# Kernel optimization log

Hardware: AMD Instinct MI355X
Metric: run time of the kernel (lower is better)

## Reference

```python
import jax, jax.numpy as jnp
import numpy as np
from jax import lax

N_HEAD = 16
SEQ = 2048
EMB = 512
D = SEQ // N_HEAD  # input_dim = 128
KSIZE = 3
EPS = 1e-5  # BatchNorm1d default eps


def setup_inputs() -> dict:
    key = jax.random.key(0)
    ks = jax.random.split(key, 5)
    inputs = jax.random.normal(ks[0], (8, SEQ, EMB), jnp.float32)
    # grouped Conv1d: groups = D, weight shape (out_ch, in_ch/groups, k) = (512, 4, 3)
    conv_w = jax.random.normal(ks[1], (EMB, EMB // D, KSIZE), jnp.float32) * 0.1
    conv_b = jax.random.normal(ks[2], (EMB,), jnp.float32) * 0.1
    gamma = jnp.ones((EMB,), jnp.float32)
    beta = jnp.zeros((EMB,), jnp.float32)
    lin_w = jax.random.normal(ks[3], (D, D), jnp.float32) * (1.0 / np.sqrt(D))
    lin_b = jax.random.normal(ks[4], (D,), jnp.float32) * 0.1
    return {"inputs": inputs, "conv_w": conv_w, "conv_b": conv_b,
            "gamma": gamma, "beta": beta, "lin_w": lin_w, "lin_b": lin_b}


def reference(inputs, conv_w, conv_b, gamma, beta, lin_w, lin_b):
    b = inputs.shape[0]
    # nlp mode: (b, S, E) -> (b*n_head, E, D)
    x = inputs.reshape(-1, EMB, D)

    # local information: grouped Conv1d (stride 1, padding 1, groups=D) + residual, GELU, BatchNorm (training stats)
    conv = lax.conv_general_dilated(
        x, conv_w, window_strides=(1,), padding=[(1, 1)],
        dimension_numbers=("NCH", "OIH", "NCH"), feature_group_count=D,
    ) + conv_b[None, :, None]
    q = jax.nn.gelu(conv + x, approximate=False)
    mu = q.mean(axis=(0, 2), keepdims=True)
    var = q.var(axis=(0, 2), keepdims=True)  # biased, as torch BN uses for normalization
    q = gamma[None, :, None] * (q - mu) * lax.rsqrt(var + EPS) + beta[None, :, None]

    # bernoulli sampling with prob=1 -> all-ones mask -> plain softmax over dim=-2 (the E axis)
    k = jax.nn.gelu(jax.nn.softmax(x, axis=1), approximate=False)

    # global information: Linear(D, D) on last dim, then GELU
    v = jax.nn.gelu(jnp.einsum("bed,od->beo", x, lin_w) + lin_b, approximate=False)

    # attention: (B', E, D) x (B', D, E) -> (B', E, E), softmax over last dim
    attn = jax.nn.softmax(
        jnp.einsum("bed,bfd->bef", q, k) / np.float32(np.sqrt(EMB)), axis=-1
    )
    out = jnp.einsum("bef,bfd->bed", attn, v)  # (B', E, D)
    return out.reshape(b, SEQ, EMB), attn
```

## Files before the change

### kernel.cpp

```cpp
#include <hip/hip_runtime.h>
#include <math.h>

#define Bn   128
#define Ech  512
#define Dd   128
#define NCNT 16384

typedef __bf16 bf16;
typedef __attribute__((ext_vector_type(8))) __bf16 bf16x8;
typedef __attribute__((ext_vector_type(4))) __bf16 bf16x4;
typedef __attribute__((ext_vector_type(4))) float f32x4;

__device__ __forceinline__ float gelu_exact(float x) {
    return 0.5f * x * (1.0f + erff(x * 0.70710678118654752f));
}

static __device__ __forceinline__ f32x4 mfma16(bf16x8 a, bf16x8 b, f32x4 c) {
    return __builtin_amdgcn_mfma_f32_16x16x32_bf16(a, b, c, 0, 0, 0);
}

__device__ __forceinline__ void stage_tile_bf16(const bf16* __restrict__ src,
                                                int src_ld, bf16* __restrict__ lds,
                                                int t)
{
    #pragma unroll
    for (int p = 0; p < 4; p++) {
        const int idx = t + 256 * p;
        const int row = idx >> 4;
        const int k16 = idx & 15;
        const float4 v = *(const float4*)((const char*)src +
                          (size_t)row * src_ld * 2 + k16 * 16);
        const unsigned byte = (unsigned)(row * 256 + k16 * 16) ^ ((row & 7) << 4);
        *(float4*)((char*)lds + byte) = v;
    }
}

__device__ __forceinline__ void stage_tile_f32(const float* __restrict__ src,
                                               int src_ld, bf16* __restrict__ lds,
                                               int t)
{
    #pragma unroll
    for (int p = 0; p < 4; p++) {
        const int idx = t + 256 * p;
        const int row = idx >> 4;
        const int k16 = idx & 15;
        const float4 a = *(const float4*)(src + (size_t)row * src_ld + k16 * 8);
        const float4 b = *(const float4*)(src + (size_t)row * src_ld + k16 * 8 + 4);
        bf16x8 o;
        o[0] = (bf16)a.x; o[1] = (bf16)a.y; o[2] = (bf16)a.z; o[3] = (bf16)a.w;
        o[4] = (bf16)b.x; o[5] = (bf16)b.y; o[6] = (bf16)b.z; o[7] = (bf16)b.w;
        const unsigned byte = (unsigned)(row * 256 + k16 * 16) ^ ((row & 7) << 4);
        *(bf16x8*)((char*)lds + byte) = o;
    }
}

__device__ __forceinline__ bf16x8 frag(const bf16* __restrict__ lds, int row, int koff)
{
    const unsigned byte = (unsigned)(row * 256 + koff * 2) ^ ((row & 7) << 4);
    return *(const bf16x8*)((const char*)lds + byte);
}

__global__ __launch_bounds__(256) void k_conv_gelu_stats(
    const float* __restrict__ x, const float* __restrict__ cw,
    const float* __restrict__ cb, bf16* __restrict__ qpre,
    float* __restrict__ csum, float* __restrict__ csumsq)
{
    __shared__ float xt[64 * 128];
    const int n  = blockIdx.y;
    const int c0 = blockIdx.x * 64;
    const float* xb = x + (size_t)n * Ech * Dd + (size_t)c0 * Dd;

    const float4* xb4 = (const float4*)xb;
    float4* xt4 = (float4*)xt;
    #pragma unroll
    for (int j = 0; j < 8; j++) xt4[threadIdx.x + 256 * j] = xb4[threadIdx.x + 256 * j];
    __syncthreads();

    const int oloc = threadIdx.x >> 2;
    const int hq   = threadIdx.x & 3;
    const int o    = c0 + oloc;
    const int gb   = oloc & ~3;

    float w[4][3];
    #pragma unroll
    for (int i = 0; i < 4; i++)
        #pragma unroll
        for (int kk = 0; kk < 3; kk++) w[i][kk] = cw[o * 12 + i * 3 + kk];
    const float bias = cb[o];

    float s = 0.f, ss = 0.f;
    bf16* qrow = qpre + (size_t)n * Ech * Dd + (size_t)o * Dd;
    #pragma unroll 4
    for (int j = 0; j < 32; j++) {
        const int h = hq + 4 * j;
        float acc = bias;
        #pragma unroll
        for (int i = 0; i < 4; i++) {
            const float* row = &xt[(gb + i) * 128];
            const float xm = (h > 0)   ? row[h - 1] : 0.f;
            const float xc = row[h];
            const float xp = (h < 127) ? row[h + 1] : 0.f;
            acc = fmaf(xm, w[i][0], acc);
            acc = fmaf(xc, w[i][1], acc);
            acc = fmaf(xp, w[i][2], acc);
        }
        acc += xt[oloc * 128 + h];
        const float g = gelu_exact(acc);
        qrow[h] = (bf16)g;
        s += g; ss = fmaf(g, g, ss);
    }
    s  += __shfl_xor(s, 1);  s  += __shfl_xor(s, 2);
    ss += __shfl_xor(ss, 1); ss += __shfl_xor(ss, 2);
    if (hq == 0) { atomicAdd(&csum[o], s); atomicAdd(&csumsq[o], ss); }
}

__global__ void k_stats_final(const float* __restrict__ csum,
                              const float* __restrict__ csumsq,
                              const float* __restrict__ gamma,
                              const float* __restrict__ beta,
                              float* __restrict__ scale, float* __restrict__ shift)
{
    const int c = threadIdx.x;
    if (c < Ech) {
        const float mu   = csum[c]   * (1.0f / NCNT);
        const float var  = csumsq[c] * (1.0f / NCNT) - mu * mu;
        const float rstd = rsqrtf(var + 1e-5f);
        const float sc   = gamma[c] * rstd;
        scale[c] = sc;
        shift[c] = beta[c] - mu * sc;
    }
}

__global__ __launch_bounds__(256) void k_softmax_e_gelu_v2(
    const float* __restrict__ x, bf16* __restrict__ kout,
    float* __restrict__ ksum)
{
    __shared__ float4 red[32][8];
    const int n  = blockIdx.y;
    const int qd = blockIdx.x;
    const int t  = threadIdx.x;
    const int d4 = t & 7;
    const int eg = t >> 3;
    const float* xb = x + (size_t)n * Ech * Dd + qd * 32 + d4 * 4;

    float4 vb[16];
    float4 m4 = {-3e38f, -3e38f, -3e38f, -3e38f};
    #pragma unroll
    for (int j = 0; j < 16; j++) {
        const int e = eg + 32 * j;
        float4 v = *(const float4*)(xb + (size_t)e * Dd);
        vb[j] = v;
        m4.x = fmaxf(m4.x, v.x); m4.y = fmaxf(m4.y, v.y);
        m4.z = fmaxf(m4.z, v.z); m4.w = fmaxf(m4.w, v.w);
    }
    red[eg][d4] = m4;
    __syncthreads();
    #pragma unroll
    for (int s = 16; s >= 1; s >>= 1) {
        if (eg < s) {
            float4 a = red[eg][d4], b = red[eg + s][d4];
            a.x = fmaxf(a.x, b.x); a.y = fmaxf(a.y, b.y);
            a.z = fmaxf(a.z, b.z); a.w = fmaxf(a.w, b.w);
            red[eg][d4] = a;
        }
        __syncthreads();
    }
    m4 = red[0][d4];
    __syncthreads();

    float4 s4 = {0.f, 0.f, 0.f, 0.f};
    #pragma unroll
    for (int j = 0; j < 16; j++) {
        float4 v = vb[j];
        v.x = __expf(v.x - m4.x); v.y = __expf(v.y - m4.y);
        v.z = __expf(v.z - m4.z); v.w = __expf(v.w - m4.w);
        vb[j] = v;
        s4.x += v.x; s4.y += v.y; s4.z += v.z; s4.w += v.w;
    }
    red[eg][d4] = s4;
    __syncthreads();
    #pragma unroll
    for (int s = 16; s >= 1; s >>= 1) {
        if (eg < s) {
            float4 a = red[eg][d4], b = red[eg + s][d4];
            a.x += b.x; a.y += b.y; a.z += b.z; a.w += b.w;
            red[eg][d4] = a;
        }
        __syncthreads();
    }
    s4 = red[0][d4];
    const float4 inv4 = {1.0f / s4.x, 1.0f / s4.y, 1.0f / s4.z, 1.0f / s4.w};

    bf16* kb = kout + (size_t)n * Ech * Dd + qd * 32 + d4 * 4;
    #pragma unroll
    for (int j = 0; j < 16; j++) {
        const int e = eg + 32 * j;
        float4 p = vb[j];
        const float g0 = gelu_exact(p.x * inv4.x);
        const float g1 = gelu_exact(p.y * inv4.y);
        const float g2 = gelu_exact(p.z * inv4.z);
        const float g3 = gelu_exact(p.w * inv4.w);
        bf16x4 ov; ov[0] = (bf16)g0; ov[1] = (bf16)g1; ov[2] = (bf16)g2; ov[3] = (bf16)g3;
        *(bf16x4*)(kb + (size_t)e * Dd) = ov;
        float pp = g0 + g1 + g2 + g3;
        pp += __shfl_xor(pp, 1); pp += __shfl_xor(pp, 2); pp += __shfl_xor(pp, 4);
        if (d4 == 0) atomicAdd(&ksum[n * Ech + e], pp);
    }
}

__global__ __launch_bounds__(256) void k_qk_mfma(
    const bf16* __restrict__ qb, const bf16* __restrict__ kbuf,
    const float* __restrict__ scale, const float* __restrict__ shift,
    const float* __restrict__ ksum, float* __restrict__ attn)
{
    __shared__ bf16 As[64 * 128];
    __shared__ bf16 Bs[64 * 128];
    const int n = blockIdx.z, e0 = blockIdx.x * 64, f0 = blockIdx.y * 64;
    const int t = threadIdx.x, lane = t & 63, w = t >> 6;
    const int wr = w >> 1, wc = w & 1;
    const int lr = lane & 15, lg = lane >> 4;

    stage_tile_bf16(qb   + (size_t)n * Ech * Dd + (size_t)e0 * Dd, Dd, As, t);
    stage_tile_bf16(kbuf + (size_t)n * Ech * Dd + (size_t)f0 * Dd, Dd, Bs, t);
    __syncthreads();

    f32x4 acc[2][2] = {};
    #pragma unroll
    for (int ks = 0; ks < 4; ks++) {
        const int ko = ks * 32 + lg * 8;
        const bf16x8 a0 = frag(As, wr * 32 + lr,      ko);
        const bf16x8 a1 = frag(As, wr * 32 + 16 + lr, ko);
        const bf16x8 b0 = frag(Bs, wc * 32 + lr,      ko);
        const bf16x8 b1 = frag(Bs, wc * 32 + 16 + lr, ko);
        acc[0][0] = mfma16(a0, b0, acc[0][0]);
        acc[0][1] = mfma16(a0, b1, acc[0][1]);
        acc[1][0] = mfma16(a1, b0, acc[1][0]);
        acc[1][1] = mfma16(a1, b1, acc[1][1]);
    }

    const float rsc = 0.044194173824159216f;
    float* ab = attn + (size_t)n * Ech * Ech;
    #pragma unroll
    for (int mm = 0; mm < 2; mm++) {
        #pragma unroll
        for (int nn = 0; nn < 2; nn++) {
            const int fcol = f0 + wc * 32 + nn * 16 + lr;
            const float kf = ksum[n * Ech + fcol];
            #pragma unroll
            for (int r4 = 0; r4 < 4; r4++) {
                const int erow = e0 + wr * 32 + mm * 16 + lg * 4 + r4;
                ab[(size_t)erow * Ech + fcol] =
                    fmaf(scale[erow], acc[mm][nn][r4], shift[erow] * kf) * rsc;
            }
        }
    }
}

__global__ __launch_bounds__(256) void k_rowsoftmax(float* __restrict__ attn)
{
    const int row  = blockIdx.x * 4 + (threadIdx.x >> 6);
    const int lane = threadIdx.x & 63;
    float* rp = attn + (size_t)row * Ech;
    float4 v1 = *(float4*)(rp + lane * 4);
    float4 v2 = *(float4*)(rp + 256 + lane * 4);
    float m = fmaxf(fmaxf(fmaxf(v1.x, v1.y), fmaxf(v1.z, v1.w)),
                    fmaxf(fmaxf(v2.x, v2.y), fmaxf(v2.z, v2.w)));
    #pragma unroll
    for (int off = 32; off >= 1; off >>= 1) m = fmaxf(m, __shfl_xor(m, off));
    v1.x = __expf(v1.x - m); v1.y = __expf(v1.y - m);
    v1.z = __expf(v1.z - m); v1.w = __expf(v1.w - m);
    v2.x = __expf(v2.x - m); v2.y = __expf(v2.y - m);
    v2.z = __expf(v2.z - m); v2.w = __expf(v2.w - m);
    float s = v1.x + v1.y + v1.z + v1.w + v2.x + v2.y + v2.z + v2.w;
    #pragma unroll
    for (int off = 32; off >= 1; off >>= 1) s += __shfl_xor(s, off);
    const float inv = 1.0f / s;
    v1.x *= inv; v1.y *= inv; v1.z *= inv; v1.w *= inv;
    v2.x *= inv; v2.y *= inv; v2.z *= inv; v2.w *= inv;
    *(float4*)(rp + lane * 4) = v1;
    *(float4*)(rp + 256 + lane * 4) = v2;
}

__global__ __launch_bounds__(256) void k_vgemm_T(
    const float* __restrict__ x, const float* __restrict__ lw,
    const float* __restrict__ lb, bf16* __restrict__ vT)
{
    __shared__ bf16 As[64 * 128];
    __shared__ bf16 Bs[64 * 128];
    const int n = blockIdx.z, e0 = blockIdx.x * 64, o0 = blockIdx.y * 64;
    const int t = threadIdx.x, lane = t & 63, w = t >> 6;
    const int wr = w >> 1, wc = w & 1;
    const int lr = lane & 15, lg = lane >> 4;

    stage_tile_f32(lw + (size_t)o0 * Dd, Dd, As, t);
    stage_tile_f32(x + (size_t)n * Ech * Dd + (size_t)e0 * Dd, Dd, Bs, t);
    __syncthreads();

    f32x4 acc[2][2] = {};
    #pragma unroll
    for (int ks = 0; ks < 4; ks++) {
        const int ko = ks * 32 + lg * 8;
        const bf16x8 a0 = frag(As, wr * 32 + lr,      ko);
        const bf16x8 a1 = frag(As, wr * 32 + 16 + lr, ko);
        const bf16x8 b0 = frag(Bs, wc * 32 + lr,      ko);
        const bf16x8 b1 = frag(Bs, wc * 32 + 16 + lr, ko);
        acc[0][0] = mfma16(a0, b0, acc[0][0]);
        acc[0][1] = mfma16(a0, b1, acc[0][1]);
        acc[1][0] = mfma16(a1, b0, acc[1][0]);
        acc[1][1] = mfma16(a1, b1, acc[1][1]);
    }

    bf16* vb = vT + (size_t)n * Dd * Ech;
    #pragma unroll
    for (int mm = 0; mm < 2; mm++) {
        #pragma unroll
        for (int nn = 0; nn < 2; nn++) {
            const int ecol = e0 + wc * 32 + nn * 16 + lr;
            #pragma unroll
            for (int r4 = 0; r4 < 4; r4++) {
                const int orow = o0 + wr * 32 + mm * 16 + lg * 4 + r4;
                vb[(size_t)orow * Ech + ecol] =
                    (bf16)gelu_exact(acc[mm][nn][r4] + lb[orow]);
            }
        }
    }
}

__global__ __launch_bounds__(256) void k_outgemm_mfma(
    const float* __restrict__ attn, const bf16* __restrict__ vT,
    float* __restrict__ out)
{
    __shared__ bf16 As[64 * 128];
    __shared__ bf16 Bs[64 * 128];
    const int n = blockIdx.z, e0 = blockIdx.x * 64, d0 = blockIdx.y * 64;
    const int t = threadIdx.x, lane = t & 63, w = t >> 6;
    const int wr = w >> 1, wc = w & 1;
    const int lr = lane & 15, lg = lane >> 4;

    const float* ab = attn + (size_t)n * Ech * Ech + (size_t)e0 * Ech;
    const bf16*  vb = vT   + (size_t)n * Dd * Ech + (size_t)d0 * Ech;

    f32x4 acc[2][2] = {};
    for (int kc = 0; kc < 512; kc += 128) {
        stage_tile_f32(ab + kc, Ech, As, t);
        stage_tile_bf16(vb + kc, Ech, Bs, t);
        __syncthreads();
        #pragma unroll
        for (int ks = 0; ks < 4; ks++) {
            const int ko = ks * 32 + lg * 8;
            const bf16x8 a0 = frag(As, wr * 32 + lr,      ko);
            const bf16x8 a1 = frag(As, wr * 32 + 16 + lr, ko);
            const bf16x8 b0 = frag(Bs, wc * 32 + lr,      ko);
            const bf16x8 b1 = frag(Bs, wc * 32 + 16 + lr, ko);
            acc[0][0] = mfma16(a0, b0, acc[0][0]);
            acc[0][1] = mfma16(a0, b1, acc[0][1]);
            acc[1][0] = mfma16(a1, b0, acc[1][0]);
            acc[1][1] = mfma16(a1, b1, acc[1][1]);
        }
        __syncthreads();
    }

    float* ob = out + (size_t)n * Ech * Dd;
    #pragma unroll
    for (int mm = 0; mm < 2; mm++) {
        #pragma unroll
        for (int nn = 0; nn < 2; nn++) {
            const int dcol = d0 + wc * 32 + nn * 16 + lr;
            #pragma unroll
            for (int r4 = 0; r4 < 4; r4++) {
                const int erow = e0 + wr * 32 + mm * 16 + lg * 4 + r4;
                ob[(size_t)erow * Dd + dcol] = acc[mm][nn][r4];
            }
        }
    }
}

extern "C" void kernel_launch(void* const* d_in, const int* in_sizes, int n_in,
                              void* d_out, int out_size, void* d_ws, size_t ws_size,
                              hipStream_t stream)
{
    const float* x     = (const float*)d_in[0];
    const float* cw    = (const float*)d_in[1];
    const float* cb    = (const float*)d_in[2];
    const float* gamma = (const float*)d_in[3];
    const float* beta  = (const float*)d_in[4];
    const float* lw    = (const float*)d_in[5];
    const float* lb    = (const float*)d_in[6];

    float* out  = (float*)d_out;
    float* attn = out + (size_t)8388608;

    bf16*  qpre_bf = (bf16*)d_ws;
    bf16*  kb_bf   = qpre_bf + 8388608;
    bf16*  vT_bf   = kb_bf + 8388608;
    float* ksum    = (float*)(vT_bf + 8388608);
    float* csum    = ksum + 65536;
    float* csumsq  = csum + 512;
    float* scale   = csumsq + 512;
    float* shift   = scale + 512;

    hipMemsetAsync(ksum, 0, (65536 + 1024) * sizeof(float), stream);

    k_conv_gelu_stats<<<dim3(8, 128), 256, 0, stream>>>(x, cw, cb, qpre_bf, csum, csumsq);
    k_stats_final<<<1, 512, 0, stream>>>(csum, csumsq, gamma, beta, scale, shift);
    k_softmax_e_gelu_v2<<<dim3(4, 128), 256, 0, stream>>>(x, kb_bf, ksum);
    k_qk_mfma<<<dim3(8, 8, 128), 256, 0, stream>>>(qpre_bf, kb_bf, scale, shift, ksum, attn);
    k_rowsoftmax<<<16384, 256, 0, stream>>>(attn);
    k_vgemm_T<<<dim3(8, 2, 128), 256, 0, stream>>>(x, lw, lb, vT_bf);
    k_outgemm_mfma<<<dim3(8, 2, 128), 256, 0, stream>>>(attn, vT_bf, out);
}
```

Before: 342.9 us.

## Fuse QK GEMM, row softmax and attn@V into one attention kernel

Replaces the separate QK^T GEMM, row-softmax and output GEMM kernels with a single kernel per 64-row block. It computes full 512-wide score rows in registers, does the softmax in-register, writes attn once, and feeds bf16 probabilities from LDS straight into the PV GEMM. The BatchNorm scale/shift is now applied to Q while staging, which removes the ksum atomics and memset. This avoids the fp32 attn round trips (write, read-modify-write, read), but uses 144KB of LDS and 128 accumulator registers, so occupancy is about one block per CU. It also rounds the P fed to the second GEMM and the stored attn values to bf16.

Measured after the change: 310.6 us. 1.1x faster.

```diff
diff --git a/kernel.cpp b/kernel.cpp
--- a/kernel.cpp
+++ b/kernel.cpp
@@ -19,46 +19,7 @@
     return __builtin_amdgcn_mfma_f32_16x16x32_bf16(a, b, c, 0, 0, 0);
 }
 
-__device__ __forceinline__ void stage_tile_bf16(const bf16* __restrict__ src,
-                                                int src_ld, bf16* __restrict__ lds,
-                                                int t)
-{
-    #pragma unroll
-    for (int p = 0; p < 4; p++) {
-        const int idx = t + 256 * p;
-        const int row = idx >> 4;
-        const int k16 = idx & 15;
-        const float4 v = *(const float4*)((const char*)src +
-                          (size_t)row * src_ld * 2 + k16 * 16);
-        const unsigned byte = (unsigned)(row * 256 + k16 * 16) ^ ((row & 7) << 4);
-        *(float4*)((char*)lds + byte) = v;
-    }
-}
-
-__device__ __forceinline__ void stage_tile_f32(const float* __restrict__ src,
-                                               int src_ld, bf16* __restrict__ lds,
-                                               int t)
-{
-    #pragma unroll
-    for (int p = 0; p < 4; p++) {
-        const int idx = t + 256 * p;
-        const int row = idx >> 4;
-        const int k16 = idx & 15;
-        const float4 a = *(const float4*)(src + (size_t)row * src_ld + k16 * 8);
-        const float4 b = *(const float4*)(src + (size_t)row * src_ld + k16 * 8 + 4);
-        bf16x8 o;
-        o[0] = (bf16)a.x; o[1] = (bf16)a.y; o[2] = (bf16)a.z; o[3] = (bf16)a.w;
-        o[4] = (bf16)b.x; o[5] = (bf16)b.y; o[6] = (bf16)b.z; o[7] = (bf16)b.w;
-        const unsigned byte = (unsigned)(row * 256 + k16 * 16) ^ ((row & 7) << 4);
-        *(bf16x8*)((char*)lds + byte) = o;
-    }
-}
-
-__device__ __forceinline__ bf16x8 frag(const bf16* __restrict__ lds, int row, int koff)
-{
-    const unsigned byte = (unsigned)(row * 256 + koff * 2) ^ ((row & 7) << 4);
-    return *(const bf16x8*)((const char*)lds + byte);
-}
+#define SWZ(byte, row) ((unsigned)(byte) ^ (((unsigned)(row) & 7u) << 4))
 
 __global__ __launch_bounds__(256) void k_conv_gelu_stats(
     const float* __restrict__ x, const float* __restrict__ cw,
@@ -132,8 +93,7 @@
 }
 
 __global__ __launch_bounds__(256) void k_softmax_e_gelu_v2(
-    const float* __restrict__ x, bf16* __restrict__ kout,
-    float* __restrict__ ksum)
+    const float* __restrict__ x, bf16* __restrict__ kout)
 {
     __shared__ float4 red[32][8];
     const int n  = blockIdx.y;
@@ -196,89 +156,13 @@
     for (int j = 0; j < 16; j++) {
         const int e = eg + 32 * j;
         float4 p = vb[j];
-        const float g0 = gelu_exact(p.x * inv4.x);
-        const float g1 = gelu_exact(p.y * inv4.y);
-        const float g2 = gelu_exact(p.z * inv4.z);
-        const float g3 = gelu_exact(p.w * inv4.w);
-        bf16x4 ov; ov[0] = (bf16)g0; ov[1] = (bf16)g1; ov[2] = (bf16)g2; ov[3] = (bf16)g3;
+        bf16x4 ov;
+        ov[0] = (bf16)gelu_exact(p.x * inv4.x);
+        ov[1] = (bf16)gelu_exact(p.y * inv4.y);
+        ov[2] = (bf16)gelu_exact(p.z * inv4.z);
+        ov[3] = (bf16)gelu_exact(p.w * inv4.w);
         *(bf16x4*)(kb + (size_t)e * Dd) = ov;
-        float pp = g0 + g1 + g2 + g3;
-        pp += __shfl_xor(pp, 1); pp += __shfl_xor(pp, 2); pp += __shfl_xor(pp, 4);
-        if (d4 == 0) atomicAdd(&ksum[n * Ech + e], pp);
-    }
-}
-
-__global__ __launch_bounds__(256) void k_qk_mfma(
-    const bf16* __restrict__ qb, const bf16* __restrict__ kbuf,
-    const float* __restrict__ scale, const float* __restrict__ shift,
-    const float* __restrict__ ksum, float* __restrict__ attn)
-{
-    __shared__ bf16 As[64 * 128];
-    __shared__ bf16 Bs[64 * 128];
-    const int n = blockIdx.z, e0 = blockIdx.x * 64, f0 = blockIdx.y * 64;
-    const int t = threadIdx.x, lane = t & 63, w = t >> 6;
-    const int wr = w >> 1, wc = w & 1;
-    const int lr = lane & 15, lg = lane >> 4;
-
-    stage_tile_bf16(qb   + (size_t)n * Ech * Dd + (size_t)e0 * Dd, Dd, As, t);
-    stage_tile_bf16(kbuf + (size_t)n * Ech * Dd + (size_t)f0 * Dd, Dd, Bs, t);
-    __syncthreads();
-
-    f32x4 acc[2][2] = {};
-    #pragma unroll
-    for (int ks = 0; ks < 4; ks++) {
-        const int ko = ks * 32 + lg * 8;
-        const bf16x8 a0 = frag(As, wr * 32 + lr,      ko);
-        const bf16x8 a1 = frag(As, wr * 32 + 16 + lr, ko);
-        const bf16x8 b0 = frag(Bs, wc * 32 + lr,      ko);
-        const bf16x8 b1 = frag(Bs, wc * 32 + 16 + lr, ko);
-        acc[0][0] = mfma16(a0, b0, acc[0][0]);
-        acc[0][1] = mfma16(a0, b1, acc[0][1]);
-        acc[1][0] = mfma16(a1, b0, acc[1][0]);
-        acc[1][1] = mfma16(a1, b1, acc[1][1]);
-    }
-
-    const float rsc = 0.044194173824159216f;
-    float* ab = attn + (size_t)n * Ech * Ech;
-    #pragma unroll
-    for (int mm = 0; mm < 2; mm++) {
-        #pragma unroll
-        for (int nn = 0; nn < 2; nn++) {
-            const int fcol = f0 + wc * 32 + nn * 16 + lr;
-            const float kf = ksum[n * Ech + fcol];
-            #pragma unroll
-            for (int r4 = 0; r4 < 4; r4++) {
-                const int erow = e0 + wr * 32 + mm * 16 + lg * 4 + r4;
-                ab[(size_t)erow * Ech + fcol] =
-                    fmaf(scale[erow], acc[mm][nn][r4], shift[erow] * kf) * rsc;
-            }
-        }
-    }
-}
-
-__global__ __launch_bounds__(256) void k_rowsoftmax(float* __restrict__ attn)
-{
-    const int row  = blockIdx.x * 4 + (threadIdx.x >> 6);
-    const int lane = threadIdx.x & 63;
-    float* rp = attn + (size_t)row * Ech;
-    float4 v1 = *(float4*)(rp + lane * 4);
-    float4 v2 = *(float4*)(rp + 256 + lane * 4);
-    float m = fmaxf(fmaxf(fmaxf(v1.x, v1.y), fmaxf(v1.z, v1.w)),
-                    fmaxf(fmaxf(v2.x, v2.y), fmaxf(v2.z, v2.w)));
-    #pragma unroll
-    for (int off = 32; off >= 1; off >>= 1) m = fmaxf(m, __shfl_xor(m, off));
-    v1.x = __expf(v1.x - m); v1.y = __expf(v1.y - m);
-    v1.z = __expf(v1.z - m); v1.w = __expf(v1.w - m);
-    v2.x = __expf(v2.x - m); v2.y = __expf(v2.y - m);
-    v2.z = __expf(v2.z - m); v2.w = __expf(v2.w - m);
-    float s = v1.x + v1.y + v1.z + v1.w + v2.x + v2.y + v2.z + v2.w;
-    #pragma unroll
-    for (int off = 32; off >= 1; off >>= 1) s += __shfl_xor(s, off);
-    const float inv = 1.0f / s;
-    v1.x *= inv; v1.y *= inv; v1.z *= inv; v1.w *= inv;
-    v2.x *= inv; v2.y *= inv; v2.z *= inv; v2.w *= inv;
-    *(float4*)(rp + lane * 4) = v1;
-    *(float4*)(rp + 256 + lane * 4) = v2;
+    }
 }
 
 __global__ __launch_bounds__(256) void k_vgemm_T(
@@ -292,18 +176,39 @@
     const int wr = w >> 1, wc = w & 1;
     const int lr = lane & 15, lg = lane >> 4;
 
-    stage_tile_f32(lw + (size_t)o0 * Dd, Dd, As, t);
-    stage_tile_f32(x + (size_t)n * Ech * Dd + (size_t)e0 * Dd, Dd, Bs, t);
+    {
+        const float* sa = lw + (size_t)o0 * Dd;
+        const float* sb = x + (size_t)n * Ech * Dd + (size_t)e0 * Dd;
+        #pragma unroll
+        for (int p = 0; p < 4; p++) {
+            const int idx = t + 256 * p;
+            const int row = idx >> 4, k16 = idx & 15;
+            float4 a0 = *(const float4*)(sa + (size_t)row * Dd + k16 * 8);
+            float4 a1 = *(const float4*)(sa + (size_t)row * Dd + k16 * 8 + 4);
+            bf16x8 oa;
+            oa[0]=(bf16)a0.x; oa[1]=(bf16)a0.y; oa[2]=(bf16)a0.z; oa[3]=(bf16)a0.w;
+            oa[4]=(bf16)a1.x; oa[5]=(bf16)a1.y; oa[6]=(bf16)a1.z; oa[7]=(bf16)a1.w;
+            *(bf16x8*)((char*)As + SWZ(row * 256 + k16 * 16, row)) = oa;
+            float4 b0 = *(const float4*)(sb + (size_t)row * Dd + k16 * 8);
+            float4 b1 = *(const float4*)(sb + (size_t)row * Dd + k16 * 8 + 4);
+            bf16x8 ob;
+            ob[0]=(bf16)b0.x; ob[1]=(bf16)b0.y; ob[2]=(bf16)b0.z; ob[3]=(bf16)b0.w;
+            ob[4]=(bf16)b1.x; ob[5]=(bf16)b1.y; ob[6]=(bf16)b1.z; ob[7]=(bf16)b1.w;
+            *(bf16x8*)((char*)Bs + SWZ(row * 256 + k16 * 16, row)) = ob;
+        }
+    }
     __syncthreads();
 
     f32x4 acc[2][2] = {};
     #pragma unroll
     for (int ks = 0; ks < 4; ks++) {
         const int ko = ks * 32 + lg * 8;
-        const bf16x8 a0 = frag(As, wr * 32 + lr,      ko);
-        const bf16x8 a1 = frag(As, wr * 32 + 16 + lr, ko);
-        const bf16x8 b0 = frag(Bs, wc * 32 + lr,      ko);
-        const bf16x8 b1 = frag(Bs, wc * 32 + 16 + lr, ko);
+        const int ra0 = wr * 32 + lr, ra1 = wr * 32 + 16 + lr;
+        const int rb0 = wc * 32 + lr, rb1 = wc * 32 + 16 + lr;
+        const bf16x8 a0 = *(const bf16x8*)((char*)As + SWZ(ra0 * 256 + ko * 2, ra0));
+        const bf16x8 a1 = *(const bf16x8*)((char*)As + SWZ(ra1 * 256 + ko * 2, ra1));
+        const bf16x8 b0 = *(const bf16x8*)((char*)Bs + SWZ(rb0 * 256 + ko * 2, rb0));
+        const bf16x8 b1 = *(const bf16x8*)((char*)Bs + SWZ(rb1 * 256 + ko * 2, rb1));
         acc[0][0] = mfma16(a0, b0, acc[0][0]);
         acc[0][1] = mfma16(a0, b1, acc[0][1]);
         acc[1][0] = mfma16(a1, b0, acc[1][0]);
@@ -326,53 +231,175 @@
     }
 }
 
-__global__ __launch_bounds__(256) void k_outgemm_mfma(
-    const float* __restrict__ attn, const bf16* __restrict__ vT,
+#define QS_OFF 0
+#define KS_OFF 16384
+#define PS_OFF 16384
+#define VS_OFF 81920
+#define LDS_TOTAL 147456
+
+__global__ __launch_bounds__(256) void k_attn_fused(
+    const bf16* __restrict__ qpre, const bf16* __restrict__ kbuf,
+    const bf16* __restrict__ vT, const float* __restrict__ scale,
+    const float* __restrict__ shift, float* __restrict__ attn,
     float* __restrict__ out)
 {
-    __shared__ bf16 As[64 * 128];
-    __shared__ bf16 Bs[64 * 128];
-    const int n = blockIdx.z, e0 = blockIdx.x * 64, d0 = blockIdx.y * 64;
+    __shared__ char lds[LDS_TOTAL];
+    const int n = blockIdx.y, e0 = blockIdx.x * 64;
     const int t = threadIdx.x, lane = t & 63, w = t >> 6;
-    const int wr = w >> 1, wc = w & 1;
     const int lr = lane & 15, lg = lane >> 4;
 
-    const float* ab = attn + (size_t)n * Ech * Ech + (size_t)e0 * Ech;
-    const bf16*  vb = vT   + (size_t)n * Dd * Ech + (size_t)d0 * Ech;
-
-    f32x4 acc[2][2] = {};
-    for (int kc = 0; kc < 512; kc += 128) {
-        stage_tile_f32(ab + kc, Ech, As, t);
-        stage_tile_bf16(vb + kc, Ech, Bs, t);
-        __syncthreads();
-        #pragma unroll
-        for (int ks = 0; ks < 4; ks++) {
-            const int ko = ks * 32 + lg * 8;
-            const bf16x8 a0 = frag(As, wr * 32 + lr,      ko);
-            const bf16x8 a1 = frag(As, wr * 32 + 16 + lr, ko);
-            const bf16x8 b0 = frag(Bs, wc * 32 + lr,      ko);
-            const bf16x8 b1 = frag(Bs, wc * 32 + 16 + lr, ko);
-            acc[0][0] = mfma16(a0, b0, acc[0][0]);
-            acc[0][1] = mfma16(a0, b1, acc[0][1]);
-            acc[1][0] = mfma16(a1, b0, acc[1][0]);
-            acc[1][1] = mfma16(a1, b1, acc[1][1]);
-        }
-        __syncthreads();
+    {
+        const bf16* src = qpre + (size_t)n * Ech * Dd + (size_t)e0 * Dd;
+        #pragma unroll
+        for (int p = 0; p < 4; p++) {
+            const int idx = t + 256 * p;
+            const int row = idx >> 4, k16 = idx & 15;
+            bf16x8 v = *(const bf16x8*)(src + row * Dd + k16 * 8);
+            const float sc = scale[e0 + row], sh = shift[e0 + row];
+            bf16x8 o;
+            #pragma unroll
+            for (int j = 0; j < 8; j++) o[j] = (bf16)fmaf((float)v[j], sc, sh);
+            *(bf16x8*)(lds + QS_OFF + SWZ(row * 256 + k16 * 16, row)) = o;
+        }
+    }
+    {
+        const bf16* src = kbuf + (size_t)n * Ech * Dd;
+        #pragma unroll
+        for (int p = 0; p < 32; p++) {
+            const int idx = t + 256 * p;
+            const int row = idx >> 4, k16 = idx & 15;
+            float4 v = *(const float4*)(src + row * Dd + k16 * 8);
+            *(float4*)(lds + KS_OFF + SWZ(row * 256 + k16 * 16, row)) = v;
+        }
+    }
+    __syncthreads();
+
+    f32x4 acc[32];
+    #pragma unroll
+    for (int i = 0; i < 32; i++) acc[i] = (f32x4){0.f, 0.f, 0.f, 0.f};
+    #pragma unroll
+    for (int ks = 0; ks < 4; ks++) {
+        const int arow = w * 16 + lr;
+        const int ko = ks * 32 + lg * 8;
+        const bf16x8 a = *(const bf16x8*)(lds + QS_OFF + SWZ(arow * 256 + ko * 2, arow));
+        #pragma unroll
+        for (int ft = 0; ft < 32; ft++) {
+            const int brow = ft * 16 + lr;
+            const bf16x8 b = *(const bf16x8*)(lds + KS_OFF + SWZ(brow * 256 + ko * 2, brow));
+            acc[ft] = mfma16(a, b, acc[ft]);
+        }
+    }
+    __syncthreads();
+
+    const float rsc = 0.044194173824159216f;
+    float m[4] = {-3e38f, -3e38f, -3e38f, -3e38f};
+    #pragma unroll
+    for (int ft = 0; ft < 32; ft++)
+        #pragma unroll
+        for (int r4 = 0; r4 < 4; r4++) m[r4] = fmaxf(m[r4], acc[ft][r4]);
+    #pragma unroll
+    for (int off = 1; off <= 8; off <<= 1)
+        #pragma unroll
+        for (int r4 = 0; r4 < 4; r4++) m[r4] = fmaxf(m[r4], __shfl_xor(m[r4], off));
+
+    float s[4] = {0.f, 0.f, 0.f, 0.f};
+    #pragma unroll
+    for (int ft = 0; ft < 32; ft++)
+        #pragma unroll
+        for (int r4 = 0; r4 < 4; r4++) {
+            const float p = __expf((acc[ft][r4] - m[r4]) * rsc);
+            acc[ft][r4] = p;
+            s[r4] += p;
+        }
+    #pragma unroll
+    for (int off = 1; off <= 8; off <<= 1)
+        #pragma unroll
+        for (int r4 = 0; r4 < 4; r4++) s[r4] += __shfl_xor(s[r4], off);
+    float inv[4];
+    #pragma unroll
+    for (int r4 = 0; r4 < 4; r4++) inv[r4] = 1.0f / s[r4];
+
+    #pragma unroll
+    for (int ft = 0; ft < 32; ft++)
+        #pragma unroll
+        for (int r4 = 0; r4 < 4; r4++) {
+            const int row = w * 16 + lg * 4 + r4;
+            const int col = ft * 16 + lr;
+            *(bf16*)(lds + PS_OFF + SWZ(row * 1024 + col * 2, row)) =
+                (bf16)(acc[ft][r4] * inv[r4]);
+        }
+
+    const bf16* vsrc = vT + (size_t)n * Dd * Ech;
+    #pragma unroll
+    for (int p = 0; p < 16; p++) {
+        const int idx = t + 256 * p;
+        const int row = idx >> 5, c16 = idx & 31;
+        float4 v = *(const float4*)(vsrc + (size_t)row * Ech + c16 * 8);
+        *(float4*)(lds + VS_OFF + SWZ(row * 512 + c16 * 16, row)) = v;
+    }
+    __syncthreads();
+
+    f32x4 acc2[8];
+    #pragma unroll
+    for (int i = 0; i < 8; i++) acc2[i] = (f32x4){0.f, 0.f, 0.f, 0.f};
+    #pragma unroll
+    for (int kf = 0; kf < 8; kf++) {
+        const int arow = w * 16 + lr;
+        const int fcol = kf * 32 + lg * 8;
+        const bf16x8 a = *(const bf16x8*)(lds + PS_OFF + SWZ(arow * 1024 + fcol * 2, arow));
+        #pragma unroll
+        for (int dt = 0; dt < 8; dt++) {
+            const int brow = dt * 16 + lr;
+            const bf16x8 b = *(const bf16x8*)(lds + VS_OFF + SWZ(brow * 512 + fcol * 2, brow));
+            acc2[dt] = mfma16(a, b, acc2[dt]);
+        }
+    }
+
+    {
+        float* ab = attn + (size_t)n * Ech * Ech + (size_t)e0 * Ech;
+        #pragma unroll
+        for (int p = 0; p < 32; p++) {
+            const int idx = t + 256 * p;
+            const int row = idx >> 7, c4 = idx & 127;
+            bf16x4 pv = *(const bf16x4*)(lds + PS_OFF + SWZ(row * 1024 + c4 * 8, row));
+            float4 o = {(float)pv[0], (float)pv[1], (float)pv[2], (float)pv[3]};
+            *(float4*)(ab + (size_t)row * Ech + c4 * 4) = o;
+        }
+    }
+    __syncthreads();
+
+    #pragma unroll
+    for (int p = 0; p < 16; p++) {
+        const int idx = t + 256 * p;
+        const int row = idx >> 5, c16 = idx & 31;
+        float4 v = *(const float4*)(vsrc + (size_t)row * Ech + 256 + c16 * 8);
+        *(float4*)(lds + VS_OFF + SWZ(row * 512 + c16 * 16, row)) = v;
+    }
+    __syncthreads();
+
+    #pragma unroll
+    for (int kf = 0; kf < 8; kf++) {
+        const int arow = w * 16 + lr;
+        const int fcol = 256 + kf * 32 + lg * 8;
+        const bf16x8 a = *(const bf16x8*)(lds + PS_OFF + SWZ(arow * 1024 + fcol * 2, arow));
+        #pragma unroll
+        for (int dt = 0; dt < 8; dt++) {
+            const int brow = dt * 16 + lr;
+            const int vcol = kf * 32 + lg * 8;
+            const bf16x8 b = *(const bf16x8*)(lds + VS_OFF + SWZ(brow * 512 + vcol * 2, brow));
+            acc2[dt] = mfma16(a, b, acc2[dt]);
+        }
     }
 
     float* ob = out + (size_t)n * Ech * Dd;
     #pragma unroll
-    for (int mm = 0; mm < 2; mm++) {
-        #pragma unroll
-        for (int nn = 0; nn < 2; nn++) {
-            const int dcol = d0 + wc * 32 + nn * 16 + lr;
-            #pragma unroll
-            for (int r4 = 0; r4 < 4; r4++) {
-                const int erow = e0 + wr * 32 + mm * 16 + lg * 4 + r4;
-                ob[(size_t)erow * Dd + dcol] = acc[mm][nn][r4];
-            }
-        }
-    }
+    for (int dt = 0; dt < 8; dt++)
+        #pragma unroll
+        for (int r4 = 0; r4 < 4; r4++) {
+            const int erow = e0 + w * 16 + lg * 4 + r4;
+            const int dcol = dt * 16 + lr;
+            ob[(size_t)erow * Dd + dcol] = acc2[dt][r4];
+        }
 }
 
 extern "C" void kernel_launch(void* const* d_in, const int* in_sizes, int n_in,
@@ -393,19 +420,17 @@
     bf16*  qpre_bf = (bf16*)d_ws;
     bf16*  kb_bf   = qpre_bf + 8388608;
     bf16*  vT_bf   = kb_bf + 8388608;
-    float* ksum    = (float*)(vT_bf + 8388608);
-    float* csum    = ksum + 65536;
+    float* csum    = (float*)(vT_bf + 8388608);
     float* csumsq  = csum + 512;
     float* scale   = csumsq + 512;
     float* shift   = scale + 512;
 
-    hipMemsetAsync(ksum, 0, (65536 + 1024) * sizeof(float), stream);
+    hipMemsetAsync(csum, 0, 2 * 512 * sizeof(float), stream);
 
     k_conv_gelu_stats<<<dim3(8, 128), 256, 0, stream>>>(x, cw, cb, qpre_bf, csum, csumsq);
     k_stats_final<<<1, 512, 0, stream>>>(csum, csumsq, gamma, beta, scale, shift);
-    k_softmax_e_gelu_v2<<<dim3(4, 128), 256, 0, stream>>>(x, kb_bf, ksum);
-    k_qk_mfma<<<dim3(8, 8, 128), 256, 0, stream>>>(qpre_bf, kb_bf, scale, shift, ksum, attn);
-    k_rowsoftmax<<<16384, 256, 0, stream>>>(attn);
+    k_softmax_e_gelu_v2<<<dim3(4, 128), 256, 0, stream>>>(x, kb_bf);
     k_vgemm_T<<<dim3(8, 2, 128), 256, 0, stream>>>(x, lw, lb, vT_bf);
-    k_outgemm_mfma<<<dim3(8, 2, 128), 256, 0, stream>>>(attn, vT_bf, out);
-}
+    k_attn_fused<<<dim3(8, 128), 256, 0, stream>>>(
+        qpre_bf, kb_bf, vT_bf, scale, shift, attn, out);
+}
```
